# Kernel tuning notes

Measured on AMD Instinct MI355X. Metric: run time of the kernel, lower is better.

## Reference

```python
import jax, jax.numpy as jnp
import numpy as np

# Config (BERT-base with T5-style shared relative attention bias)
B, S, D, H, F, V, L = 16, 512, 768, 12, 3072, 30522, 12
DH = D // H
MAXREL = 128  # bias table has 2*MAXREL+1 = 257 buckets
EPS = 1e-12


def layer_norm(x, w, b):
    mu = jnp.mean(x, axis=-1, keepdims=True)
    var = jnp.mean(jnp.square(x - mu), axis=-1, keepdims=True)
    return (x - mu) * jax.lax.rsqrt(var + EPS) * w + b


def setup_inputs() -> dict:
    key = jax.random.key(0)
    ks = jax.random.split(key, 16)
    s = 0.02
    inp = {
        "input_ids": jax.random.randint(ks[0], (B, S), 0, V),
        "attention_mask": jnp.ones((B, S), jnp.float32),
        "word_emb": jax.random.normal(ks[1], (V, D), jnp.float32) * s,
        "pos_emb": jax.random.normal(ks[2], (S, D), jnp.float32) * s,
        "emb_ln_w": jnp.ones((D,), jnp.float32),
        "emb_ln_b": jnp.zeros((D,), jnp.float32),
        "rel_bias_table": jax.random.normal(ks[3], (2 * MAXREL + 1, H), jnp.float32) * s,
        "Wq": jax.random.normal(ks[4], (L, D, D), jnp.float32) * s,
        "bq": jnp.zeros((L, D), jnp.float32),
        "Wk": jax.random.normal(ks[5], (L, D, D), jnp.float32) * s,
        "bk": jnp.zeros((L, D), jnp.float32),
        "Wv": jax.random.normal(ks[6], (L, D, D), jnp.float32) * s,
        "bv": jnp.zeros((L, D), jnp.float32),
        "Wo": jax.random.normal(ks[7], (L, D, D), jnp.float32) * s,
        "bo": jnp.zeros((L, D), jnp.float32),
        "attn_ln_w": jnp.ones((L, D), jnp.float32),
        "attn_ln_b": jnp.zeros((L, D), jnp.float32),
        "Wi": jax.random.normal(ks[8], (L, F, D), jnp.float32) * s,
        "bi": jnp.zeros((L, F), jnp.float32),
        "Wd": jax.random.normal(ks[9], (L, D, F), jnp.float32) * s,
        "bd": jnp.zeros((L, D), jnp.float32),
        "out_ln_w": jnp.ones((L, D), jnp.float32),
        "out_ln_b": jnp.zeros((L, D), jnp.float32),
    }
    return inp


def _encoder(input_ids, attention_mask, word_emb, pos_emb, emb_ln_w, emb_ln_b,
             rel_bias_table, Wq, bq, Wk, bk, Wv, bv, Wo, bo, attn_ln_w, attn_ln_b,
             Wi, bi, Wd, bd, out_ln_w, out_ln_b):
    b, s = input_ids.shape
    # Embeddings: word + learned absolute position, then LayerNorm
    h = word_emb[input_ids] + pos_emb[:s][None, :, :]
    h = layer_norm(h, emb_ln_w, emb_ln_b)

    # Shared relative position bias: [H, S, S]
    pos = jnp.arange(s)
    rel = jnp.clip(pos[None, :] - pos[:, None], -MAXREL, MAXREL) + MAXREL
    rel_bias = jnp.transpose(rel_bias_table[rel], (2, 0, 1))[None]  # [1,H,S,S]

    # Additive attention mask: [B,1,1,S]
    add_mask = (1.0 - attention_mask)[:, None, None, :] * -10000.0
    scale = 1.0 / np.sqrt(DH)

    def step(h, p):
        wq, bq_, wk, bk_, wv, bv_, wo, bo_, lw1, lb1, wi, bi_, wd, bd_, lw2, lb2 = p
        q = (h @ wq.T + bq_).reshape(b, s, H, DH)
        k = (h @ wk.T + bk_).reshape(b, s, H, DH)
        v = (h @ wv.T + bv_).reshape(b, s, H, DH)
        scores = jnp.einsum('bqhd,bkhd->bhqk', q, k) * scale + rel_bias + add_mask
        attn = jax.nn.softmax(scores, axis=-1)
        ctx = jnp.einsum('bhqk,bkhd->bqhd', attn, v).reshape(b, s, D)
        h1 = layer_norm(h + (ctx @ wo.T + bo_), lw1, lb1)
        inter = jax.nn.gelu(h1 @ wi.T + bi_, approximate=False)
        h2 = layer_norm(h1 + (inter @ wd.T + bd_), lw2, lb2)
        return h2, None

    params = (Wq, bq, Wk, bk, Wv, bv, Wo, bo, attn_ln_w, attn_ln_b,
              Wi, bi, Wd, bd, out_ln_w, out_ln_b)
    h, _ = jax.lax.scan(step, h, params)
    return h


def reference(input_ids, attention_mask, word_emb, pos_emb, emb_ln_w, emb_ln_b,
              rel_bias_table, Wq, bq, Wk, bk, Wv, bv, Wo, bo, attn_ln_w, attn_ln_b,
              Wi, bi, Wd, bd, out_ln_w, out_ln_b):
    return _encoder(input_ids, attention_mask, word_emb, pos_emb, emb_ln_w, emb_ln_b,
                    rel_bias_table, Wq, bq, Wk, bk, Wv, bv, Wo, bo, attn_ln_w, attn_ln_b,
                    Wi, bi, Wd, bd, out_ln_w, out_ln_b)
```

## Files before the change

kernel.cpp:

```cpp
#include <hip/hip_runtime.h>
#include <hip/hip_bf16.h>
#include <cstdint>
#include <cstddef>

#define BB 16
#define SS 512
#define DD 768
#define HH 12
#define FF 3072
#define LL 12
#define DHD 64
#define MM (BB*SS)
#define LOG2E 1.4426950408889634f

typedef __attribute__((ext_vector_type(8))) short bf16x8;
typedef __attribute__((ext_vector_type(4))) float f32x4;

__device__ __forceinline__ ushort f2bf(float f) {
  return __bfloat16_as_ushort(__float2bfloat16(f));
}
__device__ __forceinline__ float bf2f(ushort u) {
  union { uint32_t u; float f; } x; x.u = (uint32_t)u << 16;
  return x.f;
}

__device__ __forceinline__ void glds16(const ushort* g, ushort* l) {
  __builtin_amdgcn_global_load_lds((__attribute__((address_space(1))) void*)g,
                                   (__attribute__((address_space(3))) void*)l,
                                   16, 0, 0);
}

__device__ __forceinline__ float gelu_t(float v) {
  const float v2 = v * v;
  const float u = v * (-1.5957691216f - 0.0713548163f * v2);
  return v / (1.f + __expf(u));
}

__global__ __launch_bounds__(256)
void convw6(const float* __restrict__ s0, const float* __restrict__ s1,
            const float* __restrict__ s2, const float* __restrict__ s3,
            const float* __restrict__ s4, const float* __restrict__ s5,
            ushort* __restrict__ dA, ushort* __restrict__ dB, int perD, int perF)
{
  const int y = blockIdx.y;
  const int per = (y < 4) ? perD : perF;
  const int i = (blockIdx.x * 256 + threadIdx.x) * 4;
  if (i >= per) return;
  const float* s = y == 0 ? s0 : y == 1 ? s1 : y == 2 ? s2 : y == 3 ? s3 : y == 4 ? s4 : s5;
  ushort* dst = (y < 4) ? (dA + (size_t)y * perD) : (dB + (size_t)(y - 4) * perF);
  const float4 v = *(const float4*)(s + i);
  ushort4 o;
  o.x = f2bf(v.x); o.y = f2bf(v.y); o.z = f2bf(v.z); o.w = f2bf(v.w);
  *(ushort4*)(dst + i) = o;
}

__global__ __launch_bounds__(256)
void embed_ln_kernel(const int* __restrict__ ids, const float* __restrict__ wemb,
                     const float* __restrict__ pemb, const float* __restrict__ g,
                     const float* __restrict__ bt, ushort* __restrict__ hb)
{
  const int row = blockIdx.x;
  const int s = row & (SS - 1);
  const int id = ids[row];
  const float* wp = wemb + (size_t)id * DD;
  const float* pp = pemb + (size_t)s * DD;
  const int tid = threadIdx.x;
  float v[3]; float sum = 0.f, sq = 0.f;
#pragma unroll
  for (int j = 0; j < 3; ++j) {
    int e = tid + j * 256;
    v[j] = wp[e] + pp[e];
    sum += v[j]; sq += v[j] * v[j];
  }
  __shared__ float red[2][4];
#pragma unroll
  for (int off = 32; off >= 1; off >>= 1) { sum += __shfl_xor(sum, off); sq += __shfl_xor(sq, off); }
  const int lane = tid & 63, wid = tid >> 6;
  if (lane == 0) { red[0][wid] = sum; red[1][wid] = sq; }
  __syncthreads();
  sum = red[0][0] + red[0][1] + red[0][2] + red[0][3];
  sq  = red[1][0] + red[1][1] + red[1][2] + red[1][3];
  const float mean = sum * (1.f / DD);
  const float var  = sq  * (1.f / DD) - mean * mean;
  const float rstd = rsqrtf(var + 1e-12f);
  const size_t base = (size_t)row * DD;
#pragma unroll
  for (int j = 0; j < 3; ++j) {
    int e = tid + j * 256;
    float o = (v[j] - mean) * rstd * g[e] + bt[e];
    hb[base + e] = f2bf(o);
  }
}

template<bool FOUT>
__global__ __launch_bounds__(256)
void add_ln2_kernel(const ushort* __restrict__ res, const ushort* __restrict__ p0,
                    const ushort* __restrict__ p1, const float* __restrict__ g,
                    const float* __restrict__ bt, ushort* __restrict__ hb,
                    float* __restrict__ fout)
{
  const int row = blockIdx.x;
  const int tid = threadIdx.x;
  const size_t base = (size_t)row * DD;
  float v[3]; float sum = 0.f, sq = 0.f;
#pragma unroll
  for (int j = 0; j < 3; ++j) {
    int e = tid + j * 256;
    v[j] = bf2f(res[base + e]) + bf2f(p0[base + e]) + bf2f(p1[base + e]);
    sum += v[j]; sq += v[j] * v[j];
  }
  __shared__ float red[2][4];
#pragma unroll
  for (int off = 32; off >= 1; off >>= 1) { sum += __shfl_xor(sum, off); sq += __shfl_xor(sq, off); }
  const int lane = tid & 63, wid = tid >> 6;
  if (lane == 0) { red[0][wid] = sum; red[1][wid] = sq; }
  __syncthreads();
  sum = red[0][0] + red[0][1] + red[0][2] + red[0][3];
  sq  = red[1][0] + red[1][1] + red[1][2] + red[1][3];
  const float mean = sum * (1.f / DD);
  const float var  = sq  * (1.f / DD) - mean * mean;
  const float rstd = rsqrtf(var + 1e-12f);
#pragma unroll
  for (int j = 0; j < 3; ++j) {
    int e = tid + j * 256;
    float o = (v[j] - mean) * rstd * g[e] + bt[e];
    hb[base + e] = f2bf(o);
    if (FOUT) fout[base + e] = o;
  }
}

template<int EPI, bool TRV>
__global__ __launch_bounds__(256, 4)
void gemm_ker(const ushort* __restrict__ A,
              const ushort* __restrict__ B0, const ushort* __restrict__ B1,
              const ushort* __restrict__ B2,
              const float* __restrict__ bias0, const float* __restrict__ bias1,
              const float* __restrict__ bias2,
              void* __restrict__ C0, void* __restrict__ C1, void* __restrict__ C2,
              int Kdim, int nblk)
{
  __shared__ ushort As[2][128 * 32];
  __shared__ ushort Bs[2][128 * 32];

  const int id = blockIdx.y * gridDim.x + blockIdx.x;
  const int x = id & 7;
  const int r = id >> 3;
  const int bm = x * 8 + (r & 7);
  const int bnAll = r >> 3;
  const int sub = bnAll / nblk;
  const int bn = bnAll - sub * nblk;

  const ushort* Bw  = sub == 0 ? B0 : (sub == 1 ? B1 : B2);
  const float* bias = sub == 0 ? bias0 : (sub == 1 ? bias1 : bias2);
  const int Ndim = nblk * 128;

  const int tid = threadIdx.x;
  const int l = tid & 63, w = tid >> 6;
  const int wm = w >> 1, wn = w & 1;
  const int fr = l & 15, fg = l >> 4;

  const int srow_in = l >> 2;
  const int gks = ((l & 3) ^ ((l >> 3) & 3)) * 8;
  const ushort* Agl0 = A  + (size_t)(bm * 128 + w * 16 + srow_in) * Kdim + gks;
  const ushort* Agl1 = Agl0 + (size_t)64 * Kdim;
  const ushort* Bgl0 = Bw + (size_t)(bn * 128 + w * 16 + srow_in) * Kdim + gks;
  const ushort* Bgl1 = Bgl0 + (size_t)64 * Kdim;

  auto stage = [&](int b, int kt) {
    const int ko = kt * 32;
    ushort* al = &As[b][w * 64 * 8];
    ushort* bl = &Bs[b][w * 64 * 8];
    glds16(Agl0 + ko, al);
    glds16(Agl1 + ko, al + 256 * 8);
    glds16(Bgl0 + ko, bl);
    glds16(Bgl1 + ko, bl + 256 * 8);
  };

  const int se = (fg ^ ((fr >> 1) & 3)) * 8;

  f32x4 acc[4][4];
#pragma unroll
  for (int i = 0; i < 4; ++i)
#pragma unroll
    for (int j = 0; j < 4; ++j) acc[i][j] = f32x4{0.f, 0.f, 0.f, 0.f};

  stage(0, 0);
  __syncthreads();

  const int nk = Kdim >> 5;
  int cur = 0;
  for (int kt = 0; kt < nk; ++kt) {
    if (kt + 1 < nk) stage(cur ^ 1, kt + 1);

    bf16x8 af[4], bfv[4];
#pragma unroll
    for (int i = 0; i < 4; ++i)
      af[i]  = *(const bf16x8*)&As[cur][(wm * 64 + i * 16 + fr) * 32 + se];
#pragma unroll
    for (int j = 0; j < 4; ++j)
      bfv[j] = *(const bf16x8*)&Bs[cur][(wn * 64 + j * 16 + fr) * 32 + se];

    __builtin_amdgcn_s_setprio(1);
#pragma unroll
    for (int i = 0; i < 4; ++i)
#pragma unroll
      for (int j = 0; j < 4; ++j)
        acc[i][j] = __builtin_amdgcn_mfma_f32_16x16x32_bf16(bfv[j], af[i], acc[i][j], 0, 0, 0);
    __builtin_amdgcn_s_setprio(0);

    __syncthreads();
    cur ^= 1;
  }

#pragma unroll
  for (int i = 0; i < 4; ++i) {
    const int row_g = bm * 128 + wm * 64 + i * 16 + fr;
#pragma unroll
    for (int j = 0; j < 4; ++j) {
      const int col = bn * 128 + wn * 64 + j * 16 + fg * 4;
      const float4 bv4 = *(const float4*)&bias[col];
      const float v0 = acc[i][j][0] + bv4.x;
      const float v1 = acc[i][j][1] + bv4.y;
      const float v2 = acc[i][j][2] + bv4.z;
      const float v3 = acc[i][j][3] + bv4.w;
      if (TRV && sub == 2) {
        const int b_ = row_g >> 9, s_ = row_g & 511;
        const int h_ = col >> 6, d0 = col & 63;
        ushort* vp = (ushort*)C2 + (((size_t)(b_ * HH + h_) * DHD + d0) * SS + s_);
        vp[0] = f2bf(v0); vp[SS] = f2bf(v1); vp[2 * SS] = f2bf(v2); vp[3 * SS] = f2bf(v3);
      } else if (EPI == 2) {
        ushort4 o4;
        o4.x = f2bf(gelu_t(v0)); o4.y = f2bf(gelu_t(v1));
        o4.z = f2bf(gelu_t(v2)); o4.w = f2bf(gelu_t(v3));
        *(ushort4*)&((ushort*)C0)[(size_t)row_g * Ndim + col] = o4;
      } else {
        void* Cout = sub == 0 ? C0 : (sub == 1 ? C1 : C2);
        ushort4 o4;
        o4.x = f2bf(v0); o4.y = f2bf(v1); o4.z = f2bf(v2); o4.w = f2bf(v3);
        *(ushort4*)&((ushort*)Cout)[(size_t)row_g * Ndim + col] = o4;
      }
    }
  }
}

__global__ __launch_bounds__(256, 4)
void gemm_sk(const ushort* __restrict__ A, const ushort* __restrict__ Bw,
             const float* __restrict__ bias, ushort* __restrict__ P0,
             ushort* __restrict__ P1, int Kdim)
{
  __shared__ ushort As[2][128 * 32];
  __shared__ ushort Bs[2][128 * 32];

  const int id = blockIdx.y * gridDim.x + blockIdx.x;
  const int x = id & 7;
  const int r = id >> 3;
  const int bm = x * 8 + (r & 7);
  const int rest = r >> 3;
  const int bn = rest >> 1;
  const int sk = rest & 1;

  const int Kh = Kdim >> 1;

  const int tid = threadIdx.x;
  const int l = tid & 63, w = tid >> 6;
  const int wm = w >> 1, wn = w & 1;
  const int fr = l & 15, fg = l >> 4;

  const int srow_in = l >> 2;
  const int gks = ((l & 3) ^ ((l >> 3) & 3)) * 8;
  const ushort* Agl0 = A  + (size_t)(bm * 128 + w * 16 + srow_in) * Kdim + sk * Kh + gks;
  const ushort* Agl1 = Agl0 + (size_t)64 * Kdim;
  const ushort* Bgl0 = Bw + (size_t)(bn * 128 + w * 16 + srow_in) * Kdim + sk * Kh + gks;
  const ushort* Bgl1 = Bgl0 + (size_t)64 * Kdim;

  auto stage = [&](int b, int kt) {
    const int ko = kt * 32;
    ushort* al = &As[b][w * 64 * 8];
    ushort* bl = &Bs[b][w * 64 * 8];
    glds16(Agl0 + ko, al);
    glds16(Agl1 + ko, al + 256 * 8);
    glds16(Bgl0 + ko, bl);
    glds16(Bgl1 + ko, bl + 256 * 8);
  };

  const int se = (fg ^ ((fr >> 1) & 3)) * 8;

  f32x4 acc[4][4];
#pragma unroll
  for (int i = 0; i < 4; ++i)
#pragma unroll
    for (int j = 0; j < 4; ++j) acc[i][j] = f32x4{0.f, 0.f, 0.f, 0.f};

  stage(0, 0);
  __syncthreads();

  const int nk = Kh >> 5;
  int cur = 0;
  for (int kt = 0; kt < nk; ++kt) {
    if (kt + 1 < nk) stage(cur ^ 1, kt + 1);

    bf16x8 af[4], bfv[4];
#pragma unroll
    for (int i = 0; i < 4; ++i)
      af[i]  = *(const bf16x8*)&As[cur][(wm * 64 + i * 16 + fr) * 32 + se];
#pragma unroll
    for (int j = 0; j < 4; ++j)
      bfv[j] = *(const bf16x8*)&Bs[cur][(wn * 64 + j * 16 + fr) * 32 + se];

    __builtin_amdgcn_s_setprio(1);
#pragma unroll
    for (int i = 0; i < 4; ++i)
#pragma unroll
      for (int j = 0; j < 4; ++j)
        acc[i][j] = __builtin_amdgcn_mfma_f32_16x16x32_bf16(bfv[j], af[i], acc[i][j], 0, 0, 0);
    __builtin_amdgcn_s_setprio(0);

    __syncthreads();
    cur ^= 1;
  }

  ushort* P = sk ? P1 : P0;
  const float bs = sk ? 0.f : 1.f;
#pragma unroll
  for (int i = 0; i < 4; ++i) {
    const int row_g = bm * 128 + wm * 64 + i * 16 + fr;
#pragma unroll
    for (int j = 0; j < 4; ++j) {
      const int col = bn * 128 + wn * 64 + j * 16 + fg * 4;
      const float4 bv4 = *(const float4*)&bias[col];
      ushort4 o4;
      o4.x = f2bf(acc[i][j][0] + bv4.x * bs);
      o4.y = f2bf(acc[i][j][1] + bv4.y * bs);
      o4.z = f2bf(acc[i][j][2] + bv4.z * bs);
      o4.w = f2bf(acc[i][j][3] + bv4.w * bs);
      *(ushort4*)&P[(size_t)row_g * DD + col] = o4;
    }
  }
}

__global__ __launch_bounds__(512, 2)
void attn_kernel(const ushort* __restrict__ qb, const ushort* __restrict__ kb,
                 const ushort* __restrict__ vt, const float* __restrict__ relt,
                 const float* __restrict__ amask, ushort* __restrict__ ctxb)
{
  __shared__ ushort Kl[2][128 * 32];
  __shared__ ushort Vl[4][64 * 32];
  __shared__ ushort Plq[4][128 * 32];
  __shared__ float am_lds[512];
  __shared__ float rel_lds[1024];

  const int tid = threadIdx.x, lane = tid & 63, w = tid >> 6;

  int lin = blockIdx.y * gridDim.x + blockIdx.x;
  lin = (lin & 7) * 96 + (lin >> 3);
  const int qt = lin & 3;
  const int bh = lin >> 2;
  const int b = bh / HH, h = bh - b * HH;
  const int fr = lane & 15, fg = lane >> 4;

  am_lds[tid] = (1.0f - amask[b * SS + tid]) * (-10000.0f * LOG2E);
  {
    int d0 = tid - 512;
    d0 = max(-128, d0);
    rel_lds[tid] = relt[(d0 + 128) * HH + h] * LOG2E;
    int d1 = tid;
    d1 = min(128, d1);
    rel_lds[tid + 512] = relt[(d1 + 128) * HH + h] * LOG2E;
  }

  bf16x8 qf[2];
  {
    const int qrow = qt * 128 + w * 16 + fr;
    const ushort* p = qb + ((size_t)(b * SS + qrow) * DD) + h * DHD + fg * 8;
    qf[0] = *(const bf16x8*)p;
    qf[1] = *(const bf16x8*)(p + 32);
  }

  f32x4 o[4];
  float mrow[4], lrow[4];
#pragma unroll
  for (int r = 0; r < 4; ++r) { mrow[r] = -1e30f; lrow[r] = 0.f; }
#pragma unroll
  for (int d = 0; d < 4; ++d) o[d] = f32x4{0.f, 0.f, 0.f, 0.f};

  const int skr  = tid >> 2;
  const int kalf = (tid & 3) >> 1;
  const int ks0  = 2 * (tid & 1);
  const int kmw  = (skr >> 1) & 3;
  const int vrow = tid >> 3;
  const int vq   = (tid & 7) >> 1;
  const int vs0  = 2 * (tid & 1);
  const int vmw  = (vrow >> 1) & 3;
  const ushort* vgl = vt + ((size_t)bh * DHD + vrow) * SS + (tid & 7) * 16;

  const int sse = (fg ^ ((fr >> 1) & 3)) * 8;

  const int qg0 = qt * 128 + w * 16;

  int4 kr0, kr1, vr0, vr1;
  auto load_tile = [&](int kt) {
    const size_t gbase = ((size_t)(b * SS + kt * 128 + skr) * DD) + h * DHD + (tid & 3) * 16;
    kr0 = *(const int4*)(kb + gbase);
    kr1 = *(const int4*)(kb + gbase + 8);
    const ushort* vp = vgl + kt * 128;
    vr0 = *(const int4*)(vp);
    vr1 = *(const int4*)(vp + 8);
  };

  load_tile(0);

  for (int kt = 0; kt < 4; ++kt) {
    __syncthreads();
    *(int4*)&Kl[kalf][skr * 32 + ((ks0 ^ kmw) * 8)]       = kr0;
    *(int4*)&Kl[kalf][skr * 32 + (((ks0 + 1) ^ kmw) * 8)] = kr1;
    *(int4*)&Vl[vq][vrow * 32 + ((vs0 ^ vmw) * 8)]        = vr0;
    *(int4*)&Vl[vq][vrow * 32 + (((vs0 + 1) ^ vmw) * 8)]  = vr1;
    __syncthreads();

    if (kt + 1 < 4) load_tile(kt + 1);

    float sv[8][4];
    __builtin_amdgcn_s_setprio(1);
#pragma unroll
    for (int kc = 0; kc < 8; ++kc) {
      f32x4 s = f32x4{0.f, 0.f, 0.f, 0.f};
      const int kr = kc * 16 + fr;
      bf16x8 kf0 = *(const bf16x8*)&Kl[0][kr * 32 + sse];
      bf16x8 kf1 = *(const bf16x8*)&Kl[1][kr * 32 + sse];
      s = __builtin_amdgcn_mfma_f32_16x16x32_bf16(qf[0], kf0, s, 0, 0, 0);
      s = __builtin_amdgcn_mfma_f32_16x16x32_bf16(qf[1], kf1, s, 0, 0, 0);
      const int col = kt * 128 + kc * 16 + fr;
      const float am = am_lds[col];
      const int ridx = col - qg0 - fg * 4 + 512;
#pragma unroll
      for (int r = 0; r < 4; ++r)
        sv[kc][r] = s[r] * (0.125f * LOG2E) + rel_lds[ridx - r] + am;
    }
    __builtin_amdgcn_s_setprio(0);

    float ef[4];
#pragma unroll
    for (int r = 0; r < 4; ++r) {
      float tmax = sv[0][r];
#pragma unroll
      for (int kc = 1; kc < 8; ++kc) tmax = fmaxf(tmax, sv[kc][r]);
#pragma unroll
      for (int off = 1; off < 16; off <<= 1) tmax = fmaxf(tmax, __shfl_xor(tmax, off));
      const float mnew = fmaxf(mrow[r], tmax);
      ef[r] = exp2f(mrow[r] - mnew);
      float psum = 0.f;
      const int prow = w * 16 + fg * 4 + r;
      const int mp = (prow >> 1) & 3;
#pragma unroll
      for (int kc = 0; kc < 8; ++kc) {
        float p = exp2f(sv[kc][r] - mnew);
        psum += p;
        const int slot_ = 2 * (kc & 1) + (fr >> 3);
        Plq[kc >> 1][prow * 32 + ((slot_ ^ mp) * 8) + (fr & 7)] = f2bf(p);
      }
#pragma unroll
      for (int off = 1; off < 16; off <<= 1) psum += __shfl_xor(psum, off);
      lrow[r] = lrow[r] * ef[r] + psum;
      mrow[r] = mnew;
    }
#pragma unroll
    for (int dc = 0; dc < 4; ++dc)
#pragma unroll
      for (int r = 0; r < 4; ++r) o[dc][r] *= ef[r];
    __syncthreads();

    __builtin_amdgcn_s_setprio(1);
#pragma unroll
    for (int dc = 0; dc < 4; ++dc) {
      const int vr_ = dc * 16 + fr;
      const int pr_ = w * 16 + fr;
#pragma unroll
      for (int ks = 0; ks < 4; ++ks) {
        bf16x8 pf = *(const bf16x8*)&Plq[ks][pr_ * 32 + sse];
        bf16x8 vf = *(const bf16x8*)&Vl[ks][vr_ * 32 + sse];
        o[dc] = __builtin_amdgcn_mfma_f32_16x16x32_bf16(pf, vf, o[dc], 0, 0, 0);
      }
    }
    __builtin_amdgcn_s_setprio(0);
  }

#pragma unroll
  for (int dc = 0; dc < 4; ++dc)
#pragma unroll
    for (int r = 0; r < 4; ++r) {
      const int qg = qt * 128 + w * 16 + fg * 4 + r;
      const float v = o[dc][r] / lrow[r];
      ctxb[((size_t)(b * SS + qg) * DD) + h * DHD + dc * 16 + fr] = f2bf(v);
    }
}

extern "C" void kernel_launch(void* const* d_in, const int* in_sizes, int n_in,
                              void* d_out, int out_size, void* d_ws, size_t ws_size,
                              hipStream_t stream) {
  const int*   ids   = (const int*)d_in[0];
  const float* amask = (const float*)d_in[1];
  const float* wemb  = (const float*)d_in[2];
  const float* pemb  = (const float*)d_in[3];
  const float* eln_w = (const float*)d_in[4];
  const float* eln_b = (const float*)d_in[5];
  const float* relt  = (const float*)d_in[6];
  const float* Wq    = (const float*)d_in[7];
  const float* bq    = (const float*)d_in[8];
  const float* Wk    = (const float*)d_in[9];
  const float* bk    = (const float*)d_in[10];
  const float* Wv    = (const float*)d_in[11];
  const float* bv    = (const float*)d_in[12];
  const float* Wo    = (const float*)d_in[13];
  const float* bo    = (const float*)d_in[14];
  const float* aln_w = (const float*)d_in[15];
  const float* aln_b = (const float*)d_in[16];
  const float* Wi    = (const float*)d_in[17];
  const float* bi    = (const float*)d_in[18];
  const float* Wd    = (const float*)d_in[19];
  const float* bd    = (const float*)d_in[20];
  const float* oln_w = (const float*)d_in[21];
  const float* oln_b = (const float*)d_in[22];

  size_t off = 0;
  auto carve = [&](size_t bytes) -> void* {
    void* r = (char*)d_ws + off;
    off += (bytes + 255) & ~(size_t)255;
    return r;
  };
  ushort* hb     = (ushort*)carve((size_t)MM * DD * 2);
  ushort* qbuf   = (ushort*)carve((size_t)MM * DD * 2);
  ushort* kbuf   = (ushort*)carve((size_t)MM * DD * 2);
  ushort* vbuf   = (ushort*)carve((size_t)MM * DD * 2);
  ushort* ctxb   = (ushort*)carve((size_t)MM * DD * 2);
  ushort* gout   = (ushort*)carve((size_t)MM * DD * 2);
  ushort* gout2  = (ushort*)carve((size_t)MM * DD * 2);
  ushort* interb = (ushort*)carve((size_t)MM * FF * 2);
  const int PD = DD * DD;
  const int PF = FF * DD;
  ushort* wBded  = (ushort*)carve((size_t)2 * PF * 2);

  ushort* wA = interb;

  embed_ln_kernel<<<MM, 256, 0, stream>>>(ids, wemb, pemb, eln_w, eln_b, hb);

  const dim3 gQKV(MM / 128, 3 * (DD / 128));
  const dim3 gSK(MM / 128, 2 * (DD / 128));
  const dim3 gF(MM / 128, FF / 128);
  const dim3 gA(SS / 128, BB * HH);
  const dim3 gC(PF / 1024, 6);

  for (int l = 0; l < LL; ++l) {
    const size_t wo  = (size_t)l * PD;
    const size_t wio = (size_t)l * PF;

    convw6<<<gC, 256, 0, stream>>>(Wq + wo, Wk + wo, Wv + wo, Wo + wo,
                                   Wi + wio, Wd + wio, wA, wBded, PD, PF);

    gemm_ker<0, true><<<gQKV, 256, 0, stream>>>(hb, wA, wA + PD, wA + 2 * PD,
                                                bq + l * DD, bk + l * DD, bv + l * DD,
                                                qbuf, kbuf, vbuf, DD, DD / 128);

    attn_kernel<<<gA, 512, 0, stream>>>(qbuf, kbuf, vbuf, relt, amask, ctxb);

    gemm_sk<<<gSK, 256, 0, stream>>>(ctxb, wA + 3 * PD, bo + l * DD, gout, gout2, DD);
    add_ln2_kernel<false><<<MM, 256, 0, stream>>>(hb, gout, gout2,
                                                  aln_w + l * DD, aln_b + l * DD,
                                                  hb, nullptr);

    gemm_ker<2, false><<<gF, 256, 0, stream>>>(hb, wBded, wBded, wBded,
                                               bi + l * FF, bi + l * FF, bi + l * FF,
                                               interb, interb, interb, DD, FF / 128);
    gemm_sk<<<gSK, 256, 0, stream>>>(interb, wBded + PF, bd + l * DD, gout, gout2, FF);

    if (l == LL - 1)
      add_ln2_kernel<true><<<MM, 256, 0, stream>>>(hb, gout, gout2,
                                                   oln_w + l * DD, oln_b + l * DD,
                                                   hb, (float*)d_out);
    else
      add_ln2_kernel<false><<<MM, 256, 0, stream>>>(hb, gout, gout2,
                                                    oln_w + l * DD, oln_b + l * DD,
                                                    hb, nullptr);
  }
}
```

Baseline: 2.924 ms.

## Use 256x256 tiles with 512 threads for QKV and FFN-up GEMMs

Replaces the 128x128-tile GEMM kernel used for the fused QKV projection and the FFN up-projection with a 256x256-tile kernel running 8 waves per block, each wave computing 128x64 of output. The larger tile doubles operand reuse per LDS load and halves global-memory traffic per output element. The cost is double the LDS (64KB), more accumulator registers, occupancy capped at 2 blocks per CU, and fewer blocks in the grid (288 and 384), which may not fill all CUs evenly. K is hardcoded to 768.

```diff
diff --git a/kernel.cpp b/kernel.cpp
--- a/kernel.cpp
+++ b/kernel.cpp
@@ -129,80 +129,75 @@
   }
 }
 
-template<int EPI, bool TRV>
-__global__ __launch_bounds__(256, 4)
-void gemm_ker(const ushort* __restrict__ A,
-              const ushort* __restrict__ B0, const ushort* __restrict__ B1,
-              const ushort* __restrict__ B2,
-              const float* __restrict__ bias0, const float* __restrict__ bias1,
-              const float* __restrict__ bias2,
-              void* __restrict__ C0, void* __restrict__ C1, void* __restrict__ C2,
-              int Kdim, int nblk)
+template<int MODE>
+__global__ __launch_bounds__(512, 2)
+void gemm256(const ushort* __restrict__ A, const ushort* __restrict__ Bbase,
+             const float* __restrict__ b0, const float* __restrict__ b1,
+             const float* __restrict__ b2,
+             ushort* __restrict__ o0, ushort* __restrict__ o1,
+             ushort* __restrict__ o2)
 {
-  __shared__ ushort As[2][128 * 32];
-  __shared__ ushort Bs[2][128 * 32];
+  __shared__ ushort As[2][256 * 32];
+  __shared__ ushort Bs[2][256 * 32];
 
   const int id = blockIdx.y * gridDim.x + blockIdx.x;
   const int x = id & 7;
   const int r = id >> 3;
-  const int bm = x * 8 + (r & 7);
-  const int bnAll = r >> 3;
-  const int sub = bnAll / nblk;
-  const int bn = bnAll - sub * nblk;
-
-  const ushort* Bw  = sub == 0 ? B0 : (sub == 1 ? B1 : B2);
-  const float* bias = sub == 0 ? bias0 : (sub == 1 ? bias1 : bias2);
-  const int Ndim = nblk * 128;
+  const int bm = x * 4 + (r & 3);
+  const int bn = r >> 2;
 
   const int tid = threadIdx.x;
-  const int l = tid & 63, w = tid >> 6;
-  const int wm = w >> 1, wn = w & 1;
-  const int fr = l & 15, fg = l >> 4;
-
-  const int srow_in = l >> 2;
-  const int gks = ((l & 3) ^ ((l >> 3) & 3)) * 8;
-  const ushort* Agl0 = A  + (size_t)(bm * 128 + w * 16 + srow_in) * Kdim + gks;
-  const ushort* Agl1 = Agl0 + (size_t)64 * Kdim;
-  const ushort* Bgl0 = Bw + (size_t)(bn * 128 + w * 16 + srow_in) * Kdim + gks;
-  const ushort* Bgl1 = Bgl0 + (size_t)64 * Kdim;
+  const int lane = tid & 63, w = tid >> 6;
+  const int wr = w >> 2, wc = w & 3;
+  const int fr = lane & 15, fg = lane >> 4;
+
+  const int sub = (MODE == 0) ? (bn / 3) : 0;
+  const ushort* Bw = (MODE == 0)
+      ? Bbase + (size_t)sub * (DD * DD) + (size_t)((bn - sub * 3) * 256) * 768
+      : Bbase + (size_t)(bn * 256) * 768;
+
+  const int srow0 = tid >> 2;
+  const int gswz = ((tid & 3) ^ ((tid >> 3) & 3)) * 8;
+  const ushort* Agl0 = A  + (size_t)(bm * 256 + srow0) * 768 + gswz;
+  const ushort* Agl1 = Agl0 + (size_t)128 * 768;
+  const ushort* Bgl0 = Bw + (size_t)srow0 * 768 + gswz;
+  const ushort* Bgl1 = Bgl0 + (size_t)128 * 768;
 
   auto stage = [&](int b, int kt) {
     const int ko = kt * 32;
-    ushort* al = &As[b][w * 64 * 8];
-    ushort* bl = &Bs[b][w * 64 * 8];
-    glds16(Agl0 + ko, al);
-    glds16(Agl1 + ko, al + 256 * 8);
-    glds16(Bgl0 + ko, bl);
-    glds16(Bgl1 + ko, bl + 256 * 8);
+    glds16(Agl0 + ko, &As[b][(w * 64) * 8]);
+    glds16(Agl1 + ko, &As[b][(512 + w * 64) * 8]);
+    glds16(Bgl0 + ko, &Bs[b][(w * 64) * 8]);
+    glds16(Bgl1 + ko, &Bs[b][(512 + w * 64) * 8]);
   };
 
   const int se = (fg ^ ((fr >> 1) & 3)) * 8;
 
-  f32x4 acc[4][4];
-#pragma unroll
-  for (int i = 0; i < 4; ++i)
+  f32x4 acc[8][4];
+#pragma unroll
+  for (int i = 0; i < 8; ++i)
 #pragma unroll
     for (int j = 0; j < 4; ++j) acc[i][j] = f32x4{0.f, 0.f, 0.f, 0.f};
 
   stage(0, 0);
   __syncthreads();
 
-  const int nk = Kdim >> 5;
+  const int nk = 24;
   int cur = 0;
   for (int kt = 0; kt < nk; ++kt) {
     if (kt + 1 < nk) stage(cur ^ 1, kt + 1);
 
-    bf16x8 af[4], bfv[4];
-#pragma unroll
-    for (int i = 0; i < 4; ++i)
-      af[i]  = *(const bf16x8*)&As[cur][(wm * 64 + i * 16 + fr) * 32 + se];
+    bf16x8 af[8], bfv[4];
 #pragma unroll
     for (int j = 0; j < 4; ++j)
-      bfv[j] = *(const bf16x8*)&Bs[cur][(wn * 64 + j * 16 + fr) * 32 + se];
+      bfv[j] = *(const bf16x8*)&Bs[cur][(wc * 64 + j * 16 + fr) * 32 + se];
+#pragma unroll
+    for (int i = 0; i < 8; ++i)
+      af[i]  = *(const bf16x8*)&As[cur][(wr * 128 + i * 16 + fr) * 32 + se];
 
     __builtin_amdgcn_s_setprio(1);
 #pragma unroll
-    for (int i = 0; i < 4; ++i)
+    for (int i = 0; i < 8; ++i)
 #pragma unroll
       for (int j = 0; j < 4; ++j)
         acc[i][j] = __builtin_amdgcn_mfma_f32_16x16x32_bf16(bfv[j], af[i], acc[i][j], 0, 0, 0);
@@ -213,31 +208,38 @@
   }
 
 #pragma unroll
-  for (int i = 0; i < 4; ++i) {
-    const int row_g = bm * 128 + wm * 64 + i * 16 + fr;
+  for (int i = 0; i < 8; ++i) {
+    const int row_g = bm * 256 + wr * 128 + i * 16 + fr;
 #pragma unroll
     for (int j = 0; j < 4; ++j) {
-      const int col = bn * 128 + wn * 64 + j * 16 + fg * 4;
-      const float4 bv4 = *(const float4*)&bias[col];
-      const float v0 = acc[i][j][0] + bv4.x;
-      const float v1 = acc[i][j][1] + bv4.y;
-      const float v2 = acc[i][j][2] + bv4.z;
-      const float v3 = acc[i][j][3] + bv4.w;
-      if (TRV && sub == 2) {
-        const int b_ = row_g >> 9, s_ = row_g & 511;
-        const int h_ = col >> 6, d0 = col & 63;
-        ushort* vp = (ushort*)C2 + (((size_t)(b_ * HH + h_) * DHD + d0) * SS + s_);
-        vp[0] = f2bf(v0); vp[SS] = f2bf(v1); vp[2 * SS] = f2bf(v2); vp[3 * SS] = f2bf(v3);
-      } else if (EPI == 2) {
+      if (MODE == 0) {
+        const int csub = (bn - sub * 3) * 256 + wc * 64 + j * 16 + fg * 4;
+        const float* bias = sub == 0 ? b0 : (sub == 1 ? b1 : b2);
+        const float4 bv4 = *(const float4*)&bias[csub];
+        const float v0 = acc[i][j][0] + bv4.x;
+        const float v1 = acc[i][j][1] + bv4.y;
+        const float v2 = acc[i][j][2] + bv4.z;
+        const float v3 = acc[i][j][3] + bv4.w;
+        if (sub < 2) {
+          ushort* out = sub == 0 ? o0 : o1;
+          ushort4 o4;
+          o4.x = f2bf(v0); o4.y = f2bf(v1); o4.z = f2bf(v2); o4.w = f2bf(v3);
+          *(ushort4*)&out[(size_t)row_g * DD + csub] = o4;
+        } else {
+          const int b_ = row_g >> 9, s_ = row_g & 511;
+          const int h_ = csub >> 6, d0 = csub & 63;
+          ushort* vp = o2 + (((size_t)(b_ * HH + h_) * DHD + d0) * SS + s_);
+          vp[0] = f2bf(v0); vp[SS] = f2bf(v1); vp[2 * SS] = f2bf(v2); vp[3 * SS] = f2bf(v3);
+        }
+      } else {
+        const int col = bn * 256 + wc * 64 + j * 16 + fg * 4;
+        const float4 bv4 = *(const float4*)&b0[col];
         ushort4 o4;
-        o4.x = f2bf(gelu_t(v0)); o4.y = f2bf(gelu_t(v1));
-        o4.z = f2bf(gelu_t(v2)); o4.w = f2bf(gelu_t(v3));
-        *(ushort4*)&((ushort*)C0)[(size_t)row_g * Ndim + col] = o4;
-      } else {
-        void* Cout = sub == 0 ? C0 : (sub == 1 ? C1 : C2);
-        ushort4 o4;
-        o4.x = f2bf(v0); o4.y = f2bf(v1); o4.z = f2bf(v2); o4.w = f2bf(v3);
-        *(ushort4*)&((ushort*)Cout)[(size_t)row_g * Ndim + col] = o4;
+        o4.x = f2bf(gelu_t(acc[i][j][0] + bv4.x));
+        o4.y = f2bf(gelu_t(acc[i][j][1] + bv4.y));
+        o4.z = f2bf(gelu_t(acc[i][j][2] + bv4.z));
+        o4.w = f2bf(gelu_t(acc[i][j][3] + bv4.w));
+        *(ushort4*)&o0[(size_t)row_g * FF + col] = o4;
       }
     }
   }
@@ -543,9 +545,9 @@
 
   embed_ln_kernel<<<MM, 256, 0, stream>>>(ids, wemb, pemb, eln_w, eln_b, hb);
 
-  const dim3 gQKV(MM / 128, 3 * (DD / 128));
+  const dim3 gQKV(MM / 256, 9);
   const dim3 gSK(MM / 128, 2 * (DD / 128));
-  const dim3 gF(MM / 128, FF / 128);
+  const dim3 gF(MM / 256, FF / 256);
   const dim3 gA(SS / 128, BB * HH);
   const dim3 gC(PF / 1024, 6);
 
@@ -556,9 +558,9 @@
     convw6<<<gC, 256, 0, stream>>>(Wq + wo, Wk + wo, Wv + wo, Wo + wo,
                                    Wi + wio, Wd + wio, wA, wBded, PD, PF);
 
-    gemm_ker<0, true><<<gQKV, 256, 0, stream>>>(hb, wA, wA + PD, wA + 2 * PD,
-                                                bq + l * DD, bk + l * DD, bv + l * DD,
-                                                qbuf, kbuf, vbuf, DD, DD / 128);
+    gemm256<0><<<gQKV, 512, 0, stream>>>(hb, wA,
+                                         bq + l * DD, bk + l * DD, bv + l * DD,
+                                         qbuf, kbuf, vbuf);
 
     attn_kernel<<<gA, 512, 0, stream>>>(qbuf, kbuf, vbuf, relt, amask, ctxb);
 
@@ -567,9 +569,9 @@
                                                   aln_w + l * DD, aln_b + l * DD,
                                                   hb, nullptr);
 
-    gemm_ker<2, false><<<gF, 256, 0, stream>>>(hb, wBded, wBded, wBded,
-                                               bi + l * FF, bi + l * FF, bi + l * FF,
-                                               interb, interb, interb, DD, FF / 128);
+    gemm256<1><<<gF, 512, 0, stream>>>(hb, wBded,
+                                       bi + l * FF, nullptr, nullptr,
+                                       interb, nullptr, nullptr);
     gemm_sk<<<gSK, 256, 0, stream>>>(interb, wBded + PF, bd + l * DD, gout, gout2, FF);
 
     if (l == LL - 1)
```

Result: slower. 3.302 ms (+12.9%).
